# Kernel optimization log

Measured on AMD Instinct MI355X. Metric: run time of the kernel, lower is better.

Reference implementation:

```python
import jax, jax.numpy as jnp
import numpy as np

B, S, H, HS, D = 256, 16, 8, 128, 1024
M = H * HS  # mem_size = 1024
FORGET_BIAS = 1.0


def setup_inputs() -> dict:
    key = jax.random.key(0)
    ks = jax.random.split(key, 16)
    n = lambda k, shape, s=0.02: (jax.random.normal(k, shape, jnp.float32) * s)
    return {
        'inputs': jax.random.normal(ks[0], (B, D), jnp.float32),
        'h_state': jax.random.normal(ks[1], (B, S, M), jnp.float32),
        'm_state': jax.random.normal(ks[2], (B, S, M), jnp.float32),
        'W_emb': n(ks[3], (D, M)), 'b_emb': jnp.zeros((M,), jnp.float32),
        'W_g': n(ks[4], (M, M)), 'b_g': jnp.zeros((M,), jnp.float32),
        'W_wf': n(ks[5], (D, M)), 'W_wi': n(ks[6], (D, M)), 'W_wo': n(ks[7], (D, M)),
        'W_uf': n(ks[8], (M, M)), 'b_uf': jnp.zeros((M,), jnp.float32),
        'W_ui': n(ks[9], (M, M)), 'b_ui': jnp.zeros((M,), jnp.float32),
        'W_uo': n(ks[10], (M, M)), 'b_uo': jnp.zeros((M,), jnp.float32),
    }


def _rmc_forward(inputs, h_state, m_state, W_emb, b_emb, W_g, b_g,
                 W_wf, W_wi, W_wo, W_uf, b_uf, W_ui, b_ui, W_uo, b_uo):
    # input embedding: [B, D] -> [B, M]
    dense_inputs = inputs @ W_emb + b_emb
    # keys/values: memory with the embedded input appended as an extra slot -> [B, S+1, M]
    kv = jnp.concatenate([m_state, dense_inputs[:, None, :]], axis=1)
    # multi-head scaled dot-product attention (no q/k/v projections in AttentionMap)
    q = m_state.reshape(B, S, H, HS)
    k = kv.reshape(B, S + 1, H, HS)
    v = kv.reshape(B, S + 1, H, HS)
    scores = jnp.einsum('bqhd,bkhd->bhqk', q, k) / jnp.sqrt(jnp.asarray(HS, q.dtype))
    attn = jax.nn.softmax(scores, axis=-1)
    attended = jnp.einsum('bhqk,bkhd->bqhd', attn, v).reshape(B, S, M)

    memory_proposal = m_state + attended
    memory_proposal = (memory_proposal @ W_g + b_g) + memory_proposal

    forget_gate = jax.nn.sigmoid(h_state @ W_uf + b_uf + (inputs @ W_wf)[:, None, :])
    input_gate = jax.nn.sigmoid(h_state @ W_ui + b_ui + (inputs @ W_wi)[:, None, :])
    output_gate = jax.nn.sigmoid(h_state @ W_uo + b_uo + (inputs @ W_wo)[:, None, :])

    # NOTE: faithful to the original (including the sigmoid around m*f + bias and
    # the double-sigmoid on the input/output gates)
    new_memories = jax.nn.sigmoid(m_state * forget_gate + FORGET_BIAS) \
        + memory_proposal * jax.nn.sigmoid(input_gate)
    new_hidden = jnp.tanh(m_state) * jax.nn.sigmoid(output_gate)
    return new_memories, new_hidden


def reference(inputs, h_state, m_state, W_emb, b_emb, W_g, b_g,
              W_wf, W_wi, W_wo, W_uf, b_uf, W_ui, b_ui, W_uo, b_uo):
    return _rmc_forward(inputs, h_state, m_state, W_emb, b_emb, W_g, b_g,
                        W_wf, W_wi, W_wo, W_uf, b_uf, W_ui, b_ui, W_uo, b_uo)
```

## Files before the change

kernel.cpp:

```cpp
#include <hip/hip_runtime.h>
#include <hip/hip_bf16.h>


typedef __hip_bfloat16 bf16;
typedef __bf16 bf16x8 __attribute__((ext_vector_type(8)));
typedef float  f32x4  __attribute__((ext_vector_type(4)));
typedef unsigned short u16x8 __attribute__((ext_vector_type(8)));

__device__ __forceinline__ float b2f(bf16 x) { return __bfloat162float(x); }
__device__ __forceinline__ bf16  f2b(float x) { return __float2bfloat16(x); }
__device__ __forceinline__ unsigned short fbits(float x) {
    bf16 b = __float2bfloat16(x);
    return *(unsigned short*)&b;
}
__device__ __forceinline__ float bu2f(unsigned short u) {
    unsigned int x = ((unsigned int)u) << 16;
    float f;
    __builtin_memcpy(&f, &x, 4);
    return f;
}
__device__ __forceinline__ float sig(float x) { return 1.0f / (1.0f + __expf(-x)); }
__device__ __forceinline__ float ftanh(float x) {
    return 1.0f - 2.0f / (1.0f + __expf(2.0f * x));
}

__device__ __forceinline__ void gl_lds16(const void* g, void* l) {
    __builtin_amdgcn_global_load_lds(
        (const __attribute__((address_space(1))) void*)g,
        (__attribute__((address_space(3))) void*)l,
        16, 0, 0);
}

__global__ __launch_bounds__(256) void k_prep(
    const float* __restrict__ W_g, const float* __restrict__ W_uf,
    const float* __restrict__ W_ui, const float* __restrict__ W_uo,
    const float* __restrict__ W_emb, const float* __restrict__ W_wf,
    const float* __restrict__ W_wi, const float* __restrict__ W_wo,
    const float* __restrict__ h_state, const float* __restrict__ inputs,
    bf16* __restrict__ wt, bf16* __restrict__ hbf, float* __restrict__ part)
{
    __shared__ __align__(16) char sbuf[49152];
    const int blk = blockIdx.x;
    const int tid = threadIdx.x;

    if (blk < 256) {
        const float* Wsrc4[4] = {W_emb, W_wf, W_wi, W_wo};
        const int ks = blk & 1;
        const int mt = (blk >> 1) & 1;
        const int nt = blk >> 2;
        const int which = nt >> 4;
        const int n0 = (nt & 15) * 64;
        const int m0 = mt * 128;
        const int kbase = ks * 512;
        const float* Wsrc = Wsrc4[which];

        const int wv = tid >> 6, lane = tid & 63;
        const int mrow = lane & 15, q = lane >> 4;
        const int rb = (wv & 1) * 64, cb = (wv >> 1) * 32;

        const int arow = tid >> 4, af4 = tid & 15;
        const int kq = tid >> 4, cq = tid & 15;

        float4 aR[8], bR[4], aN[8], bN[4];

        auto LOADX = [&](int k0, float4* a, float4* b) {
            #pragma unroll
            for (int r = 0; r < 8; ++r)
                a[r] = *(const float4*)(inputs + (size_t)(m0 + r * 16 + arow) * 1024 + k0 + af4 * 4);
            const float* wp = Wsrc + (size_t)(k0 + kq * 4) * 1024 + n0 + cq * 4;
            b[0] = *(const float4*)(wp);
            b[1] = *(const float4*)(wp + 1024);
            b[2] = *(const float4*)(wp + 2048);
            b[3] = *(const float4*)(wp + 3072);
        };
        auto WRITEX = [&](char* LA, char* LB, const float4* a, const float4* b) {
            #pragma unroll
            for (int r = 0; r < 8; ++r) {
                const int row = r * 16 + arow;
                ushort4 p;
                p.x = fbits(a[r].x); p.y = fbits(a[r].y);
                p.z = fbits(a[r].z); p.w = fbits(a[r].w);
                *(ushort4*)(LA + row * 128 + ((af4 * 8) ^ ((row & 7) << 4))) = p;
            }
            const float* e0 = (const float*)&b[0];
            const float* e1 = (const float*)&b[1];
            const float* e2 = (const float*)&b[2];
            const float* e3 = (const float*)&b[3];
            #pragma unroll
            for (int j = 0; j < 4; ++j) {
                const int c = cq * 4 + j;
                ushort4 p;
                p.x = fbits(e0[j]); p.y = fbits(e1[j]);
                p.z = fbits(e2[j]); p.w = fbits(e3[j]);
                *(ushort4*)(LB + c * 128 + ((kq * 8) ^ ((c & 7) << 4))) = p;
            }
        };

        const f32x4 zero4 = {0.0f, 0.0f, 0.0f, 0.0f};
        f32x4 acc[4][2];
        #pragma unroll
        for (int i = 0; i < 4; ++i)
            #pragma unroll
            for (int j = 0; j < 2; ++j) acc[i][j] = zero4;

        LOADX(kbase, aR, bR);
        WRITEX(sbuf, sbuf + 16384, aR, bR);
        __syncthreads();

        for (int s = 0; s < 8; ++s) {
            char* LA = sbuf + (s & 1) * 24576;
            char* LB = LA + 16384;
            if (s < 7) LOADX(kbase + (s + 1) * 64, aN, bN);

            #pragma unroll
            for (int kk = 0; kk < 2; ++kk) {
                const int kb = kk * 64 + q * 16;
                bf16x8 afr[4], bfr[2];
                #pragma unroll
                for (int i = 0; i < 4; ++i) {
                    int row = rb + i * 16 + mrow;
                    afr[i] = *(const bf16x8*)(LA + row * 128 + (kb ^ ((row & 7) << 4)));
                }
                #pragma unroll
                for (int j = 0; j < 2; ++j) {
                    int n = cb + j * 16 + mrow;
                    bfr[j] = *(const bf16x8*)(LB + n * 128 + (kb ^ ((n & 7) << 4)));
                }
                #pragma unroll
                for (int i = 0; i < 4; ++i)
                    #pragma unroll
                    for (int j = 0; j < 2; ++j)
                        acc[i][j] = __builtin_amdgcn_mfma_f32_16x16x32_bf16(afr[i], bfr[j], acc[i][j], 0, 0, 0);
            }

            if (s < 7) {
                __syncthreads();
                char* LAn = sbuf + ((s + 1) & 1) * 24576;
                WRITEX(LAn, LAn + 16384, aN, bN);
                __syncthreads();
            }
        }

        float* P = part + (size_t)(ks * 4 + which) * 262144;
        #pragma unroll
        for (int j = 0; j < 2; ++j) {
            const int colp = n0 + cb + j * 16 + mrow;
            #pragma unroll
            for (int i = 0; i < 4; ++i)
                #pragma unroll
                for (int r = 0; r < 4; ++r) {
                    const int row = m0 + rb + i * 16 + q * 4 + r;
                    P[(size_t)row * 1024 + colp] = acc[i][j][r];
                }
        }
    } else if (blk < 1280) {
        const float* Ws[4] = {W_g, W_uf, W_ui, W_uo};
        const int t = blk - 256;
        const int plane = t >> 8;
        const int tt = t & 255;
        const int kb = (tt >> 4) * 64;
        const int nb = (tt & 15) * 64;
        const float* W = Ws[plane];
        bf16* Wt = wt + (size_t)plane * (1024 * 1024);
        float (*tl)[65] = (float (*)[65])sbuf;

        #pragma unroll
        for (int it = 0; it < 4; ++it) {
            int lin = it * 256 + tid;
            int kr = lin >> 4, n4 = lin & 15;
            *(float4*)&tl[kr][n4 * 4] =
                *(const float4*)(W + (size_t)(kb + kr) * 1024 + nb + n4 * 4);
        }
        __syncthreads();
        #pragma unroll
        for (int it = 0; it < 2; ++it) {
            int lin = it * 256 + tid;
            int n = lin >> 3, k8 = (lin & 7) * 8;
            u16x8 p;
            #pragma unroll
            for (int j = 0; j < 8; ++j) p[j] = fbits(tl[k8 + j][n]);
            *(u16x8*)(Wt + (size_t)(nb + n) * 1024 + kb + k8) = p;
        }
    } else {
        const int e = blk - 1280;
        size_t idx = ((size_t)e * 256 + tid) * 16;
        #pragma unroll
        for (int hh = 0; hh < 2; ++hh) {
            float4 a = *(const float4*)(h_state + idx + hh * 8);
            float4 b = *(const float4*)(h_state + idx + hh * 8 + 4);
            u16x8 p;
            p[0] = fbits(a.x); p[1] = fbits(a.y); p[2] = fbits(a.z); p[3] = fbits(a.w);
            p[4] = fbits(b.x); p[5] = fbits(b.y); p[6] = fbits(b.z); p[7] = fbits(b.w);
            *(u16x8*)(hbf + idx + hh * 8) = p;
        }
    }
}

__global__ __launch_bounds__(256) void k_attn(
    const float* __restrict__ m_state,
    const float* __restrict__ part,
    const float* __restrict__ b_emb,
    bf16* __restrict__ mp)
{
    const int b = blockIdx.x >> 3;
    const int h = blockIdx.x & 7;
    const int tid = threadIdx.x;

    __shared__ float kv[17][132];
    __shared__ float sc[16][18];

    for (int idx = tid; idx < 17 * 32; idx += 256) {
        int r = idx >> 5, d4 = idx & 31;
        float4 v;
        if (r < 16) {
            v = *(const float4*)&m_state[(size_t)(b * 16 + r) * 1024 + h * 128 + d4 * 4];
        } else {
            float4 v0 = *(const float4*)&part[(size_t)b * 1024 + h * 128 + d4 * 4];
            float4 v1 = *(const float4*)&part[(size_t)(4 * 256 + b) * 1024 + h * 128 + d4 * 4];
            float4 be = *(const float4*)&b_emb[h * 128 + d4 * 4];
            v.x = v0.x + v1.x + be.x;
            v.y = v0.y + v1.y + be.y;
            v.z = v0.z + v1.z + be.z;
            v.w = v0.w + v1.w + be.w;
        }
        *(float4*)&kv[r][d4 * 4] = v;
    }
    __syncthreads();

    for (int p = tid; p < 16 * 17; p += 256) {
        int qi = p / 17, ki = p % 17;
        float dx = 0.f, dy = 0.f, dz = 0.f, dw = 0.f;
        #pragma unroll 8
        for (int d4 = 0; d4 < 32; ++d4) {
            float4 a = *(const float4*)&kv[qi][d4 * 4];
            float4 c = *(const float4*)&kv[ki][d4 * 4];
            dx += a.x * c.x; dy += a.y * c.y; dz += a.z * c.z; dw += a.w * c.w;
        }
        sc[qi][ki] = (dx + dy + dz + dw) * 0.0883883476483184f;
    }
    __syncthreads();

    if (tid < 16) {
        float mx = -1e30f;
        for (int k = 0; k < 17; ++k) mx = fmaxf(mx, sc[tid][k]);
        float s = 0.0f;
        for (int k = 0; k < 17; ++k) { float e = __expf(sc[tid][k] - mx); sc[tid][k] = e; s += e; }
        float inv = 1.0f / s;
        for (int k = 0; k < 17; ++k) sc[tid][k] *= inv;
    }
    __syncthreads();

    for (int p = tid; p < 16 * 32; p += 256) {
        int qi = p >> 5, d4 = p & 31;
        float sx = 0.f, sy = 0.f, sz = 0.f, sw = 0.f;
        #pragma unroll
        for (int k = 0; k < 17; ++k) {
            float w = sc[qi][k];
            float4 v = *(const float4*)&kv[k][d4 * 4];
            sx += w * v.x; sy += w * v.y; sz += w * v.z; sw += w * v.w;
        }
        float4 base = *(const float4*)&kv[qi][d4 * 4];
        size_t off = (size_t)(b * 16 + qi) * 1024 + h * 128 + d4 * 4;
        mp[off + 0] = f2b(base.x + sx);
        mp[off + 1] = f2b(base.y + sy);
        mp[off + 2] = f2b(base.z + sz);
        mp[off + 3] = f2b(base.w + sw);
    }
}

__global__ __launch_bounds__(512, 2) void k_gemm_big(
    const bf16* __restrict__ hbf,
    const bf16* __restrict__ mpb,
    const bf16* __restrict__ wt,
    bf16* __restrict__ pre,
    bf16* __restrict__ preg)
{
    extern __shared__ __align__(16) char smem[];

    int bid = blockIdx.x;
    bid = (bid & 7) * 32 + (bid >> 3);
    const int by = bid & 15;
    const int ct = bid >> 4;
    const int m0 = by * 256;

    const bf16* A; const bf16* Bp; bf16* Cout; int bn0;
    if (ct < 12) {
        A = hbf;
        const int g = ct >> 2;
        bn0 = (ct & 3) * 256;
        Bp = wt + (size_t)(1 + g) * (1024 * 1024);
        Cout = pre + (size_t)g * (4096 * 1024);
    } else {
        A = mpb;
        bn0 = (ct - 12) * 256;
        Bp = wt;
        Cout = preg;
    }

    const int wv = threadIdx.x >> 6;
    const int lane = threadIdx.x & 63;
    const int r8 = lane >> 3, c8 = lane & 7;
    const int mrow = lane & 15, q = lane >> 4;
    const int wr = wv >> 2, wc = wv & 3;

    const f32x4 zero4 = {0.0f, 0.0f, 0.0f, 0.0f};
    f32x4 acc[8][4];
    #pragma unroll
    for (int i = 0; i < 8; ++i)
        #pragma unroll
        for (int j = 0; j < 4; ++j) acc[i][j] = zero4;

    auto STAGE = [&](int buf, int k0) {
        char* sA = smem + buf * 65536;
        char* sB = sA + 32768;
        #pragma unroll
        for (int t = 0; t < 4; ++t) {
            const int rr = wv * 32 + t * 8;
            gl_lds16(A  + (size_t)(m0  + rr + r8) * 1024 + k0 + (c8 ^ r8) * 8, sA + rr * 128);
            gl_lds16(Bp + (size_t)(bn0 + rr + r8) * 1024 + k0 + (c8 ^ r8) * 8, sB + rr * 128);
        }
    };

    STAGE(0, 0);

    #pragma unroll 2
    for (int step = 0; step < 16; ++step) {
        const int cur = step & 1;
        if (step < 15) {
            STAGE(cur ^ 1, (step + 1) * 64);
            asm volatile("s_waitcnt vmcnt(8)" ::: "memory");
        } else {
            asm volatile("s_waitcnt vmcnt(0)" ::: "memory");
        }
        __builtin_amdgcn_s_barrier();
        __builtin_amdgcn_sched_barrier(0);

        const char* sA = smem + cur * 65536;
        const char* sB = sA + 32768;
        #pragma unroll
        for (int kk = 0; kk < 2; ++kk) {
            const int kb = kk * 64 + q * 16;
            bf16x8 afr[8], bfr[4];
            #pragma unroll
            for (int i = 0; i < 8; ++i) {
                const int row = wr * 128 + i * 16 + mrow;
                afr[i] = *(const bf16x8*)(sA + row * 128 + (kb ^ ((row & 7) << 4)));
            }
            #pragma unroll
            for (int j = 0; j < 4; ++j) {
                const int n = wc * 64 + j * 16 + mrow;
                bfr[j] = *(const bf16x8*)(sB + n * 128 + (kb ^ ((n & 7) << 4)));
            }
            #pragma unroll
            for (int i = 0; i < 8; ++i)
                #pragma unroll
                for (int j = 0; j < 4; ++j)
                    acc[i][j] = __builtin_amdgcn_mfma_f32_16x16x32_bf16(afr[i], bfr[j], acc[i][j], 0, 0, 0);
        }
        __builtin_amdgcn_sched_barrier(0);
        __builtin_amdgcn_s_barrier();
    }

    bf16* sC = (bf16*)smem;
    const int CS = 264;
    #pragma unroll
    for (int chunk = 0; chunk < 2; ++chunk) {
        __syncthreads();
        if (wr == chunk) {
            #pragma unroll
            for (int i = 0; i < 8; ++i)
                #pragma unroll
                for (int j = 0; j < 4; ++j)
                    #pragma unroll
                    for (int r = 0; r < 4; ++r) {
                        const int row = i * 16 + q * 4 + r;
                        const int col = wc * 64 + j * 16 + mrow;
                        sC[row * CS + col] = f2b(acc[i][j][r]);
                    }
        }
        __syncthreads();
        #pragma unroll
        for (int ps = 0; ps < 8; ++ps) {
            const int row = ps * 16 + (threadIdx.x >> 5);
            const int cc = (threadIdx.x & 31) * 8;
            u16x8 v = *(const u16x8*)(sC + row * CS + cc);
            *(u16x8*)(Cout + (size_t)(m0 + chunk * 128 + row) * 1024 + bn0 + cc) = v;
        }
    }
}

__global__ __launch_bounds__(256) void k_epi(
    const float* __restrict__ m_state,
    const bf16* __restrict__ mpb,
    const bf16* __restrict__ preg,
    const bf16* __restrict__ pre,
    const float* __restrict__ part,
    const float* __restrict__ b_g, const float* __restrict__ b_uf,
    const float* __restrict__ b_ui, const float* __restrict__ b_uo,
    float* __restrict__ out_mem, float* __restrict__ out_hid)
{
    const size_t idx = ((size_t)blockIdx.x * 256 + threadIdx.x) * 8;
    const int row = (int)(idx >> 10);
    const int col = (int)(idx & 1023);
    const int b = row >> 4;
    const size_t po = (size_t)b * 1024 + col;

    u16x8 mp8 = *(const u16x8*)(mpb + idx);
    u16x8 pg8 = *(const u16x8*)(preg + idx);
    u16x8 pf8 = *(const u16x8*)(pre + idx);
    u16x8 pi8 = *(const u16x8*)(pre + 4194304 + idx);
    u16x8 po8 = *(const u16x8*)(pre + 8388608 + idx);

    float4 om[2], oh[2];
    #pragma unroll
    for (int hh = 0; hh < 2; ++hh) {
        float4 m4  = *(const float4*)(m_state + idx + hh * 4);
        float4 xfa = *(const float4*)(part + 262144 + po + hh * 4);
        float4 xfb = *(const float4*)(part + 1048576 + 262144 + po + hh * 4);
        float4 xia = *(const float4*)(part + 524288 + po + hh * 4);
        float4 xib = *(const float4*)(part + 1048576 + 524288 + po + hh * 4);
        float4 xoa = *(const float4*)(part + 786432 + po + hh * 4);
        float4 xob = *(const float4*)(part + 1048576 + 786432 + po + hh * 4);
        float4 bg4 = *(const float4*)(b_g + col + hh * 4);
        float4 bf4 = *(const float4*)(b_uf + col + hh * 4);
        float4 bi4 = *(const float4*)(b_ui + col + hh * 4);
        float4 bo4 = *(const float4*)(b_uo + col + hh * 4);

        const float* mm = (const float*)&m4;
        const float* exfa = (const float*)&xfa; const float* exfb = (const float*)&xfb;
        const float* exia = (const float*)&xia; const float* exib = (const float*)&xib;
        const float* exoa = (const float*)&xoa; const float* exob = (const float*)&xob;
        const float* ebg = (const float*)&bg4; const float* ebf = (const float*)&bf4;
        const float* ebi = (const float*)&bi4; const float* ebo = (const float*)&bo4;
        float* eom = (float*)&om[hh];
        float* eoh = (float*)&oh[hh];

        #pragma unroll
        for (int u = 0; u < 4; ++u) {
            const int e = hh * 4 + u;
            float m = mm[u];
            float mp2 = bu2f(pg8[e]) + ebg[u] + bu2f(mp8[e]);
            float fg = sig(bu2f(pf8[e]) + ebf[u] + exfa[u] + exfb[u]);
            float ig = sig(bu2f(pi8[e]) + ebi[u] + exia[u] + exib[u]);
            float og = sig(bu2f(po8[e]) + ebo[u] + exoa[u] + exob[u]);
            eom[u] = sig(m * fg + 1.0f) + mp2 * sig(ig);
            eoh[u] = ftanh(m) * sig(og);
        }
    }

    *(float4*)(out_mem + idx) = om[0];
    *(float4*)(out_mem + idx + 4) = om[1];
    *(float4*)(out_hid + idx) = oh[0];
    *(float4*)(out_hid + idx + 4) = oh[1];
}

extern "C" void kernel_launch(void* const* d_in, const int* in_sizes, int n_in,
                              void* d_out, int out_size, void* d_ws, size_t ws_size,
                              hipStream_t stream)
{
    const float* inputs  = (const float*)d_in[0];
    const float* h_state = (const float*)d_in[1];
    const float* m_state = (const float*)d_in[2];
    const float* W_emb   = (const float*)d_in[3];
    const float* b_emb   = (const float*)d_in[4];
    const float* W_g     = (const float*)d_in[5];
    const float* b_g     = (const float*)d_in[6];
    const float* W_wf    = (const float*)d_in[7];
    const float* W_wi    = (const float*)d_in[8];
    const float* W_wo    = (const float*)d_in[9];
    const float* W_uf    = (const float*)d_in[10];
    const float* b_uf    = (const float*)d_in[11];
    const float* W_ui    = (const float*)d_in[12];
    const float* b_ui    = (const float*)d_in[13];
    const float* W_uo    = (const float*)d_in[14];
    const float* b_uo    = (const float*)d_in[15];

    char* wsb = (char*)d_ws;
    float* part = (float*)wsb;
    bf16*  hbf  = (bf16*)(wsb + 8u  * 1048576u);
    bf16*  mpb  = (bf16*)(wsb + 16u * 1048576u);
    bf16*  wt   = (bf16*)(wsb + 24u * 1048576u);
    bf16*  pre  = (bf16*)(wsb + 32u * 1048576u);
    bf16*  preg = (bf16*)(wsb + 56u * 1048576u);

    float* out_mem = (float*)d_out;
    float* out_hid = out_mem + (size_t)4096 * 1024;

    k_prep<<<dim3(2304), dim3(256), 0, stream>>>(
        W_g, W_uf, W_ui, W_uo, W_emb, W_wf, W_wi, W_wo,
        h_state, inputs, wt, hbf, part);

    k_attn<<<dim3(256 * 8), dim3(256), 0, stream>>>(m_state, part, b_emb, mpb);

    k_gemm_big<<<dim3(256), dim3(512), 131072, stream>>>(hbf, mpb, wt, pre, preg);

    k_epi<<<dim3(2048), dim3(256), 0, stream>>>(
        m_state, mpb, preg, pre, part,
        b_g, b_uf, b_ui, b_uo, out_mem, out_hid);
}
```

Measured before the change: 213.6 us.

## Retile big GEMM to 128x128 blocks and drop double-buffering in prep GEMM

```diff
diff --git a/kernel.cpp b/kernel.cpp
--- a/kernel.cpp
+++ b/kernel.cpp
@@ -39,7 +39,7 @@
     const float* __restrict__ h_state, const float* __restrict__ inputs,
     bf16* __restrict__ wt, bf16* __restrict__ hbf, float* __restrict__ part)
 {
-    __shared__ __align__(16) char sbuf[49152];
+    __shared__ __align__(16) char sbuf[32768];
     const int blk = blockIdx.x;
     const int tid = threadIdx.x;
 
@@ -53,49 +53,13 @@
         const int m0 = mt * 128;
         const int kbase = ks * 512;
         const float* Wsrc = Wsrc4[which];
+        char* LA = sbuf;
+        char* LB = sbuf + 16384;
 
         const int wv = tid >> 6, lane = tid & 63;
         const int mrow = lane & 15, q = lane >> 4;
         const int rb = (wv & 1) * 64, cb = (wv >> 1) * 32;
 
-        const int arow = tid >> 4, af4 = tid & 15;
-        const int kq = tid >> 4, cq = tid & 15;
-
-        float4 aR[8], bR[4], aN[8], bN[4];
-
-        auto LOADX = [&](int k0, float4* a, float4* b) {
-            #pragma unroll
-            for (int r = 0; r < 8; ++r)
-                a[r] = *(const float4*)(inputs + (size_t)(m0 + r * 16 + arow) * 1024 + k0 + af4 * 4);
-            const float* wp = Wsrc + (size_t)(k0 + kq * 4) * 1024 + n0 + cq * 4;
-            b[0] = *(const float4*)(wp);
-            b[1] = *(const float4*)(wp + 1024);
-            b[2] = *(const float4*)(wp + 2048);
-            b[3] = *(const float4*)(wp + 3072);
-        };
-        auto WRITEX = [&](char* LA, char* LB, const float4* a, const float4* b) {
-            #pragma unroll
-            for (int r = 0; r < 8; ++r) {
-                const int row = r * 16 + arow;
-                ushort4 p;
-                p.x = fbits(a[r].x); p.y = fbits(a[r].y);
-                p.z = fbits(a[r].z); p.w = fbits(a[r].w);
-                *(ushort4*)(LA + row * 128 + ((af4 * 8) ^ ((row & 7) << 4))) = p;
-            }
-            const float* e0 = (const float*)&b[0];
-            const float* e1 = (const float*)&b[1];
-            const float* e2 = (const float*)&b[2];
-            const float* e3 = (const float*)&b[3];
-            #pragma unroll
-            for (int j = 0; j < 4; ++j) {
-                const int c = cq * 4 + j;
-                ushort4 p;
-                p.x = fbits(e0[j]); p.y = fbits(e1[j]);
-                p.z = fbits(e2[j]); p.w = fbits(e3[j]);
-                *(ushort4*)(LB + c * 128 + ((kq * 8) ^ ((c & 7) << 4))) = p;
-            }
-        };
-
         const f32x4 zero4 = {0.0f, 0.0f, 0.0f, 0.0f};
         f32x4 acc[4][2];
         #pragma unroll
@@ -103,15 +67,38 @@
             #pragma unroll
             for (int j = 0; j < 2; ++j) acc[i][j] = zero4;
 
-        LOADX(kbase, aR, bR);
-        WRITEX(sbuf, sbuf + 16384, aR, bR);
-        __syncthreads();
-
         for (int s = 0; s < 8; ++s) {
-            char* LA = sbuf + (s & 1) * 24576;
-            char* LB = LA + 16384;
-            if (s < 7) LOADX(kbase + (s + 1) * 64, aN, bN);
-
+            const int k0 = kbase + s * 64;
+            #pragma unroll
+            for (int r = 0; r < 8; ++r) {
+                int lin = r * 256 + tid;
+                int row = lin >> 4, f4 = lin & 15;
+                float4 v = *(const float4*)(inputs + (size_t)(m0 + row) * 1024 + k0 + f4 * 4);
+                ushort4 p;
+                p.x = fbits(v.x); p.y = fbits(v.y); p.z = fbits(v.z); p.w = fbits(v.w);
+                *(ushort4*)(LA + row * 128 + ((f4 * 8) ^ ((row & 7) << 4))) = p;
+            }
+            {
+                int kq = tid >> 4, cq = tid & 15;
+                const float* wp = Wsrc + (size_t)(k0 + kq * 4) * 1024 + n0 + cq * 4;
+                float4 v0 = *(const float4*)(wp);
+                float4 v1 = *(const float4*)(wp + 1024);
+                float4 v2 = *(const float4*)(wp + 2048);
+                float4 v3 = *(const float4*)(wp + 3072);
+                const float* e0 = (const float*)&v0;
+                const float* e1 = (const float*)&v1;
+                const float* e2 = (const float*)&v2;
+                const float* e3 = (const float*)&v3;
+                #pragma unroll
+                for (int j = 0; j < 4; ++j) {
+                    int c = cq * 4 + j;
+                    ushort4 p;
+                    p.x = fbits(e0[j]); p.y = fbits(e1[j]);
+                    p.z = fbits(e2[j]); p.w = fbits(e3[j]);
+                    *(ushort4*)(LB + c * 128 + ((kq * 8) ^ ((c & 7) << 4))) = p;
+                }
+            }
+            __syncthreads();
             #pragma unroll
             for (int kk = 0; kk < 2; ++kk) {
                 const int kb = kk * 64 + q * 16;
@@ -132,15 +119,8 @@
                     for (int j = 0; j < 2; ++j)
                         acc[i][j] = __builtin_amdgcn_mfma_f32_16x16x32_bf16(afr[i], bfr[j], acc[i][j], 0, 0, 0);
             }
-
-            if (s < 7) {
-                __syncthreads();
-                char* LAn = sbuf + ((s + 1) & 1) * 24576;
-                WRITEX(LAn, LAn + 16384, aN, bN);
-                __syncthreads();
-            }
-        }
-
+            __syncthreads();
+        }
         float* P = part + (size_t)(ks * 4 + which) * 262144;
         #pragma unroll
         for (int j = 0; j < 2; ++j) {
@@ -268,7 +248,7 @@
     }
 }
 
-__global__ __launch_bounds__(512, 2) void k_gemm_big(
+__global__ __launch_bounds__(256, 2) void k_gemm_big(
     const bf16* __restrict__ hbf,
     const bf16* __restrict__ mpb,
     const bf16* __restrict__ wt,
@@ -278,21 +258,21 @@
     extern __shared__ __align__(16) char smem[];
 
     int bid = blockIdx.x;
-    bid = (bid & 7) * 32 + (bid >> 3);
-    const int by = bid & 15;
-    const int ct = bid >> 4;
-    const int m0 = by * 256;
+    bid = (bid & 7) * 128 + (bid >> 3);
+    const int by = bid & 31;
+    const int ct = bid >> 5;
+    const int m0 = by * 128;
 
     const bf16* A; const bf16* Bp; bf16* Cout; int bn0;
-    if (ct < 12) {
+    if (ct < 24) {
         A = hbf;
-        const int g = ct >> 2;
-        bn0 = (ct & 3) * 256;
+        const int g = ct >> 3;
+        bn0 = (ct & 7) * 128;
         Bp = wt + (size_t)(1 + g) * (1024 * 1024);
         Cout = pre + (size_t)g * (4096 * 1024);
     } else {
         A = mpb;
-        bn0 = (ct - 12) * 256;
+        bn0 = (ct - 24) * 128;
         Bp = wt;
         Cout = preg;
     }
@@ -301,18 +281,18 @@
     const int lane = threadIdx.x & 63;
     const int r8 = lane >> 3, c8 = lane & 7;
     const int mrow = lane & 15, q = lane >> 4;
-    const int wr = wv >> 2, wc = wv & 3;
+    const int wr = wv >> 1, wc = wv & 1;
 
     const f32x4 zero4 = {0.0f, 0.0f, 0.0f, 0.0f};
-    f32x4 acc[8][4];
+    f32x4 acc[4][4];
     #pragma unroll
-    for (int i = 0; i < 8; ++i)
+    for (int i = 0; i < 4; ++i)
         #pragma unroll
         for (int j = 0; j < 4; ++j) acc[i][j] = zero4;
 
     auto STAGE = [&](int buf, int k0) {
-        char* sA = smem + buf * 65536;
-        char* sB = sA + 32768;
+        char* sA = smem + buf * 32768;
+        char* sB = sA + 16384;
         #pragma unroll
         for (int t = 0; t < 4; ++t) {
             const int rr = wv * 32 + t * 8;
@@ -335,15 +315,15 @@
         __builtin_amdgcn_s_barrier();
         __builtin_amdgcn_sched_barrier(0);
 
-        const char* sA = smem + cur * 65536;
-        const char* sB = sA + 32768;
+        const char* sA = smem + cur * 32768;
+        const char* sB = sA + 16384;
         #pragma unroll
         for (int kk = 0; kk < 2; ++kk) {
             const int kb = kk * 64 + q * 16;
-            bf16x8 afr[8], bfr[4];
-            #pragma unroll
-            for (int i = 0; i < 8; ++i) {
-                const int row = wr * 128 + i * 16 + mrow;
+            bf16x8 afr[4], bfr[4];
+            #pragma unroll
+            for (int i = 0; i < 4; ++i) {
+                const int row = wr * 64 + i * 16 + mrow;
                 afr[i] = *(const bf16x8*)(sA + row * 128 + (kb ^ ((row & 7) << 4)));
             }
             #pragma unroll
@@ -352,7 +332,7 @@
                 bfr[j] = *(const bf16x8*)(sB + n * 128 + (kb ^ ((n & 7) << 4)));
             }
             #pragma unroll
-            for (int i = 0; i < 8; ++i)
+            for (int i = 0; i < 4; ++i)
                 #pragma unroll
                 for (int j = 0; j < 4; ++j)
                     acc[i][j] = __builtin_amdgcn_mfma_f32_16x16x32_bf16(afr[i], bfr[j], acc[i][j], 0, 0, 0);
@@ -362,30 +342,24 @@
     }
 
     bf16* sC = (bf16*)smem;
-    const int CS = 264;
+    const int CS = 136;
     #pragma unroll
-    for (int chunk = 0; chunk < 2; ++chunk) {
-        __syncthreads();
-        if (wr == chunk) {
-            #pragma unroll
-            for (int i = 0; i < 8; ++i)
-                #pragma unroll
-                for (int j = 0; j < 4; ++j)
-                    #pragma unroll
-                    for (int r = 0; r < 4; ++r) {
-                        const int row = i * 16 + q * 4 + r;
-                        const int col = wc * 64 + j * 16 + mrow;
-                        sC[row * CS + col] = f2b(acc[i][j][r]);
-                    }
-        }
-        __syncthreads();
-        #pragma unroll
-        for (int ps = 0; ps < 8; ++ps) {
-            const int row = ps * 16 + (threadIdx.x >> 5);
-            const int cc = (threadIdx.x & 31) * 8;
-            u16x8 v = *(const u16x8*)(sC + row * CS + cc);
-            *(u16x8*)(Cout + (size_t)(m0 + chunk * 128 + row) * 1024 + bn0 + cc) = v;
-        }
+    for (int i = 0; i < 4; ++i)
+        #pragma unroll
+        for (int j = 0; j < 4; ++j)
+            #pragma unroll
+            for (int r = 0; r < 4; ++r) {
+                const int row = wr * 64 + i * 16 + q * 4 + r;
+                const int col = wc * 64 + j * 16 + mrow;
+                sC[row * CS + col] = f2b(acc[i][j][r]);
+            }
+    __syncthreads();
+    #pragma unroll
+    for (int ps = 0; ps < 8; ++ps) {
+        const int row = ps * 16 + (threadIdx.x >> 4);
+        const int cc = (threadIdx.x & 15) * 8;
+        u16x8 v = *(const u16x8*)(sC + row * CS + cc);
+        *(u16x8*)(Cout + (size_t)(m0 + row) * 1024 + bn0 + cc) = v;
     }
 }
 
@@ -492,7 +466,7 @@
 
     k_attn<<<dim3(256 * 8), dim3(256), 0, stream>>>(m_state, part, b_emb, mpb);
 
-    k_gemm_big<<<dim3(256), dim3(512), 131072, stream>>>(hbf, mpb, wt, pre, preg);
+    k_gemm_big<<<dim3(1024), dim3(256), 65536, stream>>>(hbf, mpb, wt, pre, preg);
 
     k_epi<<<dim3(2048), dim3(256), 0, stream>>>(
         m_state, mpb, preg, pre, part,
```

Result: slower. 221.1 us (+3.5%).
